# Kernel optimization log

Measured on AMD Instinct MI355X. Metric: run time of the kernel, lower is better.

## Reference

```python
import jax, jax.numpy as jnp
import numpy as np
from jax import lax

B, DIM, H, W = 16, 256, 32, 32
C = DIM // 4          # per-branch channels = 64
HEADS, DH = 8, 64
INNER = HEADS * DH    # 512
R = 16                # SE / CBAM channel reduction
PX = PY = 8           # learned param grid size


def _coords(n_in, n_out):
    s = jnp.linspace(0.0, n_in - 1.0, n_out)
    i0 = jnp.clip(jnp.floor(s).astype(jnp.int32), 0, max(n_in - 2, 0))
    return i0, jnp.clip(i0 + 1, 0, n_in - 1), s - i0


def resize_ac(p, out_h, out_w):
    # bilinear resize with align_corners=True; p: [..., h, w]
    y0, y1, fy = _coords(p.shape[-2], out_h)
    x0, x1, fx = _coords(p.shape[-1], out_w)
    py = p[..., y0, :] * (1.0 - fy)[:, None] + p[..., y1, :] * fy[:, None]
    return py[..., x0] * (1.0 - fx) + py[..., x1] * fx


def ln_last(x, w, b, eps=1e-5):  # torch nn.LayerNorm default eps
    m = x.mean(-1, keepdims=True)
    v = ((x - m) ** 2).mean(-1, keepdims=True)
    return (x - m) * lax.rsqrt(v + eps) * w + b


def ln_cf(x, w, b, eps=1e-6):  # channels_first ConvNeXt LayerNorm
    m = x.mean(1, keepdims=True)
    v = ((x - m) ** 2).mean(1, keepdims=True)
    return w[None, :, None, None] * ((x - m) * lax.rsqrt(v + eps)) + b[None, :, None, None]


def dwconv2d(x, w, b):  # depthwise 3x3, stride 1, pad 1
    o = lax.conv_general_dilated(x, w, (1, 1), 'SAME', dimension_numbers=('NCHW', 'OIHW', 'NCHW'), feature_group_count=x.shape[1])
    return o + b[None, :, None, None]


def dwconv1d(x, w, b):  # depthwise k=3, pad 1
    o = lax.conv_general_dilated(x, w, (1,), 'SAME', dimension_numbers=('NCH', 'OIH', 'NCH'), feature_group_count=x.shape[1])
    return o + b[None, :, None]


def pw(x, w, b):  # 1x1 conv over NCHW, w: [Cout, Cin]
    return jnp.einsum('bchw,dc->bdhw', x, w) + b[None, :, None, None]


def gelu(t):
    return jax.nn.gelu(t, approximate=False)  # torch nn.GELU default = erf


def attention(x, lnw, lnb, wqkv, wout):
    # x: [B, N, C]
    xn = ln_last(x, lnw, lnb)
    q, k, v = jnp.split(xn @ wqkv, 3, axis=-1)
    sp = lambda t: t.reshape(t.shape[0], t.shape[1], HEADS, DH).transpose(0, 2, 1, 3)
    q, k, v = sp(q), sp(k), sp(v)
    a = jax.nn.softmax(jnp.einsum('bhnd,bhmd->bhnm', q, k) * DH ** -0.5, axis=-1)
    o = jnp.einsum('bhnm,bhmd->bhnd', a, v).transpose(0, 2, 1, 3).reshape(x.shape[0], x.shape[1], INNER)
    return o @ wout


def cbam(x, fc1, fc2, sa_w):
    mlp = lambda t: jax.nn.relu(t @ fc1.T) @ fc2.T
    ca = jax.nn.sigmoid(mlp(x.mean((2, 3))) + mlp(x.max((2, 3))))
    x = x * ca[:, :, None, None]
    sp = jnp.stack([x.mean(1), x.max(1)], axis=1)  # [B,2,H,W]
    sa = lax.conv_general_dilated(sp, sa_w, (1, 1), 'SAME', dimension_numbers=('NCHW', 'OIHW', 'NCHW'))
    return x * jax.nn.sigmoid(sa)


def se(x, fc1, fc2):
    y = jax.nn.sigmoid(jax.nn.relu(x.mean((2, 3)) @ fc1.T) @ fc2.T)
    return x * y[:, :, None, None]


def setup_inputs() -> dict:
    key = jax.random.key(0)
    ks = iter(jax.random.split(key, 40))
    nrm = lambda shape, s=0.05: jax.random.normal(next(ks), shape, jnp.float32) * s
    d = {}
    d['x'] = jax.random.normal(next(ks), (B, DIM, H, W), jnp.float32)
    d['n1_w'] = jnp.ones((DIM,)); d['n1_b'] = jnp.zeros((DIM,))
    d['att_ln_w'] = jnp.ones((C,)); d['att_ln_b'] = jnp.zeros((C,))
    d['att_wqkv'] = nrm((C, 3 * INNER))
    d['att_wout'] = nrm((INNER, C))
    d['params_xy'] = jnp.ones((1, C, PX, PY))
    d['cxy_dw_w'] = nrm((C, 1, 3, 3)); d['cxy_dw_b'] = jnp.zeros((C,))
    d['cxy_pw_w'] = nrm((C, C)); d['cxy_pw_b'] = jnp.zeros((C,))
    d['ca_fc1'] = nrm((C // R, C)); d['ca_fc2'] = nrm((C, C // R))
    d['sa_w'] = nrm((1, 2, 7, 7))
    d['params_zx'] = jnp.ones((1, 1, C, PX))
    d['czx_dw_w'] = nrm((C, 1, 3)); d['czx_dw_b'] = jnp.zeros((C,))
    d['czx_pw_w'] = nrm((C, C)); d['czx_pw_b'] = jnp.zeros((C,))
    d['se_fc1'] = nrm((C // R, C)); d['se_fc2'] = nrm((C, C // R))
    d['params_zy'] = jnp.ones((1, 1, C, PY))
    d['czy_dw_w'] = nrm((C, 1, 3)); d['czy_dw_b'] = jnp.zeros((C,))
    d['czy_pw_w'] = nrm((C, C)); d['czy_pw_b'] = jnp.zeros((C,))
    d['dw_pw_w'] = nrm((C, C)); d['dw_pw_b'] = jnp.zeros((C,))
    d['dw_dw_w'] = nrm((C, 1, 3, 3)); d['dw_dw_b'] = jnp.zeros((C,))
    d['n2_w'] = jnp.ones((DIM,)); d['n2_b'] = jnp.zeros((DIM,))
    d['ldw_dw_w'] = nrm((DIM, 1, 3, 3)); d['ldw_dw_b'] = jnp.zeros((DIM,))
    d['ldw_pw_w'] = nrm((DIM, DIM)); d['ldw_pw_b'] = jnp.zeros((DIM,))
    return d


def reference(x, n1_w, n1_b, att_ln_w, att_ln_b, att_wqkv, att_wout, params_xy, cxy_dw_w, cxy_dw_b, cxy_pw_w, cxy_pw_b, ca_fc1, ca_fc2, sa_w, params_zx, czx_dw_w, czx_dw_b, czx_pw_w, czx_pw_b, se_fc1, se_fc2, params_zy, czy_dw_w, czy_dw_b, czy_pw_w, czy_pw_b, dw_pw_w, dw_pw_b, dw_dw_w, dw_dw_b, n2_w, n2_b, ldw_dw_w, ldw_dw_b, ldw_pw_w, ldw_pw_b):
    xn = ln_cf(x, n1_w, n1_b)
    x1, x2, x3, x4 = jnp.split(xn, 4, axis=1)
    Bz, Cz, Hz, Wz = x1.shape
    # branch 1: token self-attention, gated by conv'd upsampled learned grid
    t = attention(x1.transpose(0, 2, 3, 1).reshape(Bz, Hz * Wz, Cz), att_ln_w, att_ln_b, att_wqkv, att_wout)
    x1 = t.reshape(Bz, Hz, Wz, Cz).transpose(0, 3, 1, 2)
    g = pw(gelu(dwconv2d(resize_ac(params_xy, Hz, Wz), cxy_dw_w, cxy_dw_b)), cxy_pw_w, cxy_pw_b)
    x1 = x1 * g
    # branch 2: CBAM + zx gate (permute trick == broadcast over width)
    x2 = cbam(x2, ca_fc1, ca_fc2, sa_w)
    g = resize_ac(params_zx, Cz, Hz)[0]  # [1, C, H]
    g = jnp.einsum('bcl,dc->bdl', gelu(dwconv1d(g, czx_dw_w, czx_dw_b)), czx_pw_w) + czx_pw_b[None, :, None]
    x2 = x2 * g[:, :, :, None]
    # branch 3: SE + zy gate (broadcast over height)
    x3 = se(x3, se_fc1, se_fc2)
    g = resize_ac(params_zy, Cz, Wz)[0]  # [1, C, W]
    g = jnp.einsum('bcl,dc->bdl', gelu(dwconv1d(g, czy_dw_w, czy_dw_b)), czy_pw_w) + czy_pw_b[None, :, None]
    x3 = x3 * g[:, :, None, :]
    # branch 4: pointwise -> GELU -> depthwise
    x4 = dwconv2d(gelu(pw(x4, dw_pw_w, dw_pw_b)), dw_dw_w, dw_dw_b)
    out = ln_cf(jnp.concatenate([x1, x2, x3, x4], axis=1), n2_w, n2_b)
    return pw(gelu(dwconv2d(out, ldw_dw_w, ldw_dw_b)), ldw_pw_w, ldw_pw_b)
```

## Files before the change

### kernel.cpp

```cpp
#include <hip/hip_runtime.h>
#include <hip/hip_bf16.h>
#include <math.h>

#define B_     16
#define DIM_   256
#define H_     32
#define W_     32
#define HW_    1024
#define C_     64
#define HEADS_ 8
#define DH_    64
#define INNER_ 512
#define TOK_   16384

typedef unsigned short ushort_t;
typedef __bf16 bf16x8 __attribute__((ext_vector_type(8)));
typedef float  f32x4  __attribute__((ext_vector_type(4)));

#define AOFF_N1W     0
#define AOFF_N1B     256
#define AOFF_ALNW    512
#define AOFF_ALNB    576
#define AOFF_WQKV    640
#define AOFF_WOUT    98944
// ... 123 lines not shown
  int bb = pix >> 10, hw = pix & 1023;
  size_t base = (size_t)bb * (DIM_ * HW_) + hw;
  float s = 0.f, s2 = 0.f;
  for (int c = 0; c < 64; ++c) {
    float v = ldx(x, base + (size_t)(p * 64 + c) * HW_, xf);
    s += v; s2 += v * v;
  }
  ps[p][pi] = s; ps2[p][pi] = s2;
  __syncthreads();
  if (t < 64) {
    float S = ps[0][t] + ps[1][t] + ps[2][t] + ps[3][t];
    float S2 = ps2[0][t] + ps2[1][t] + ps2[2][t] + ps2[3][t];
    float mean = S * (1.0f / DIM_);
    float var = fmaxf(S2 * (1.0f / DIM_) - mean * mean, 0.f);
    int px = blockIdx.x * 64 + t;
    m1[px] = mean;
    r1[px] = rsqrtf(var + 1e-6f);
  }
}

__global__ __launch_bounds__(256) void k_ln_tok(const void* __restrict__ x, const int* __restrict__ dtf,
                                                const float* __restrict__ m1, const float* __restrict__ r1,
                                                const float* __restrict__ arena, ushort_t* __restrict__ x1ln,
                                                ushort_t* __restrict__ xn4) {
  __shared__ float ls[64 * 65];
  __shared__ float pm[4][64], pv[4][64];
  __shared__ float mt[64], rt[64];
  bool xf = dtf[0] != 0;
  int t = threadIdx.x;
  int bb = blockIdx.x >> 4, hw0 = (blockIdx.x & 15) * 64;
  #pragma unroll
  for (int i = 0; i < 16; ++i) {
    int ch = i * 4 + (t >> 6);
    int tk = t & 63;
    int tokg = bb * HW_ + hw0 + tk;
    float v = ldx(x, ((size_t)bb * DIM_ + ch) * HW_ + hw0 + tk, xf);
    ls[ch * 65 + tk] = (v - m1[tokg]) * r1[tokg] * arena[AOFF_N1W + ch] + arena[AOFF_N1B + ch];
  }
  __syncthreads();
  {
    int p = t >> 6, tk = t & 63;
    float s = 0.f, s2 = 0.f;
    #pragma unroll
    for (int c = 0; c < 16; ++c) {
      float v = ls[(p * 16 + c) * 65 + tk];
      s += v; s2 += v * v;
    }
    pm[p][tk] = s; pv[p][tk] = s2;
  }
  __syncthreads();
  if (t < 64) {
    float S = pm[0][t] + pm[1][t] + pm[2][t] + pm[3][t];
    float S2 = pv[0][t] + pv[1][t] + pv[2][t] + pv[3][t];
    float m = S * (1.0f / C_);
    float var = fmaxf(S2 * (1.0f / C_) - m * m, 0.f);
    mt[t] = m;
    rt[t] = rsqrtf(var + 1e-5f);
  }
  __syncthreads();
  {
    unsigned int* dst = (unsigned int*)x1ln;
    #pragma unroll
    for (int i = 0; i < 8; ++i) {
      int idx = i * 256 + t;
      int tok = idx >> 5, cp = idx & 31, c = cp * 2;
      float m = mt[tok], r = rt[tok];
      float v0 = (ls[c * 65 + tok] - m) * r * arena[AOFF_ALNW + c] + arena[AOFF_ALNB + c];
      float v1 = (ls[(c + 1) * 65 + tok] - m) * r * arena[AOFF_ALNW + c + 1] + arena[AOFF_ALNB + c + 1];
      int tokg = bb * HW_ + hw0 + tok;
      dst[(tokg * 64 + c) >> 1] = (unsigned int)f2us(v0) | ((unsigned int)f2us(v1) << 16);
    }
  }
  __syncthreads();
  #pragma unroll
  for (int i = 0; i < 16; ++i) {
    int ch = i * 4 + (t >> 6);
    int tk = t & 63;
    int tokg = bb * HW_ + hw0 + tk;
    float v = ldx(x, ((size_t)bb * DIM_ + 192 + ch) * HW_ + hw0 + tk, xf);
    ls[ch * 65 + tk] = (v - m1[tokg]) * r1[tokg] * arena[AOFF_N1W + 192 + ch] + arena[AOFF_N1B + 192 + ch];
  }
  __syncthreads();
  {
    unsigned int* dst = (unsigned int*)xn4;
    #pragma unroll
    for (int i = 0; i < 8; ++i) {
      int idx = i * 256 + t;
      int tok = idx >> 5, cp = idx & 31, c = cp * 2;
      float v0 = ls[c * 65 + tok];
      float v1 = ls[(c + 1) * 65 + tok];
      int tokg = bb * HW_ + hw0 + tok;
      dst[(tokg * 64 + c) >> 1] = (unsigned int)f2us(v0) | ((unsigned int)f2us(v1) << 16);
    }
  }
}

__global__ __launch_bounds__(256) void k_qkv_mfma(const ushort_t* __restrict__ x1ln,
                                                  const ushort_t* __restrict__ wqkvT,
                                                  ushort_t* __restrict__ q, ushort_t* __restrict__ k_,
                                                  ushort_t* __restrict__ v_, int tok_base) {
  int jc = blockIdx.x % 6;
  int mt = blockIdx.x / 6;
  int w = threadIdx.x >> 6, lane = threadIdx.x & 63;
  int m = lane & 15, quad = lane >> 4;
  int tok0 = mt * 64;
  bf16x8 a[4][2];
  #pragma unroll
  for (int s = 0; s < 4; ++s)
    #pragma unroll
    for (int kc = 0; kc < 2; ++kc)
      a[s][kc] = *(const bf16x8*)(x1ln + (size_t)(tok_base + tok0 + s*16 + m) * 64 + kc*32 + quad*8);
  bf16x8 bfr[4][2];
  #pragma unroll
  for (int nb = 0; nb < 4; ++nb)
    #pragma unroll
    for (int kc = 0; kc < 2; ++kc)
      bfr[nb][kc] = *(const bf16x8*)(wqkvT + (size_t)(jc*256 + w*64 + nb*16 + m) * 64 + kc*32 + quad*8);
  f32x4 cacc[4][4];
  #pragma unroll
  for (int s = 0; s < 4; ++s)
    #pragma unroll
    for (int nb = 0; nb < 4; ++nb) cacc[s][nb] = (f32x4){0.f, 0.f, 0.f, 0.f};
  #pragma unroll
  for (int kc = 0; kc < 2; ++kc)
    #pragma unroll
    for (int s = 0; s < 4; ++s)
      #pragma unroll
      for (int nb = 0; nb < 4; ++nb)
        cacc[s][nb] = __builtin_amdgcn_mfma_f32_16x16x32_bf16(a[s][kc], bfr[nb][kc], cacc[s][nb], 0, 0, 0);
  #pragma unroll
  for (int nb = 0; nb < 4; ++nb) {
    int j = jc*256 + w*64 + nb*16 + m;
    int which = j >> 9, jj = j & 511;
    int h = jj >> 6, d = jj & 63;
    ushort_t* dst = (which == 0) ? q : ((which == 1) ? k_ : v_);
    float sc = (which == 0) ? 0.125f : 1.0f;
    #pragma unroll
    for (int s = 0; s < 4; ++s)
      #pragma unroll
      for (int r = 0; r < 4; ++r) {
        int tl = tok0 + s*16 + quad*4 + r;
        int bl = tl >> 10, n = tl & 1023;
        dst[(((size_t)bl * HEADS_ + h) * 1024 + n) * 64 + d] = f2us(cacc[s][nb][r] * sc);
      }
  }
}

#define KSTR 72
__global__ __launch_bounds__(256) void k_flash_mfma(const ushort_t* __restrict__ q,
                                                    const ushort_t* __restrict__ k_,
                                                    const ushort_t* __restrict__ v_,
                                                    ushort_t* __restrict__ ao) {
  __shared__ ushort_t Kl[64 * KSTR];
  __shared__ ushort_t Vt[80 * KSTR];
  __shared__ ushort_t Pl[256 * KSTR];
  int bh = blockIdx.x >> 2;
  int qt = blockIdx.x & 3;
  int w = threadIdx.x >> 6, lane = threadIdx.x & 63;
  int m = lane & 15, quad = lane >> 4;
  const size_t bh_off = (size_t)bh * 1024 * 64;

  {
    unsigned int* vtp = (unsigned int*)&Vt[0];
    for (int i = threadIdx.x; i < 16 * (KSTR / 2); i += 256) {
      int row = i / (KSTR / 2);
      vtp[64 * (KSTR / 2) + i] = (row == 0) ? 0x3F803F80u : 0u;
    }
  }

  bf16x8 aq[4][2];
  #pragma unroll
  for (int s = 0; s < 4; ++s)
    #pragma unroll
    for (int kc = 0; kc < 2; ++kc)
      aq[s][kc] = *(const bf16x8*)(q + bh_off + (size_t)(qt*256 + w*64 + s*16 + m) * 64 + kc*32 + quad*8);

  f32x4 oacc[4][4];
  f32x4 lsum[4];
  #pragma unroll
  for (int s = 0; s < 4; ++s) {
    #pragma unroll
    for (int i = 0; i < 4; ++i) oacc[s][i] = (f32x4){0.f, 0.f, 0.f, 0.f};
    lsum[s] = (f32x4){0.f, 0.f, 0.f, 0.f};
  }

  __syncthreads();
  bf16x8 bvo0 = *(const bf16x8*)&Vt[(64 + m) * KSTR + quad*8];
  bf16x8 bvo1 = *(const bf16x8*)&Vt[(64 + m) * KSTR + 32 + quad*8];

  int kkey = threadIdx.x & 63;
  int kd0  = (threadIdx.x >> 6) * 16;
  int vkey = (threadIdx.x & 31) * 2;
  int vd0  = (threadIdx.x >> 5) * 8;

  for (int kt = 0; kt < 16; ++kt) {
    __syncthreads();
    {
      const uint4* src = (const uint4*)(k_ + bh_off + (size_t)(kt*64 + kkey)*64 + kd0);
      uint4 u0 = src[0], u1 = src[1];
      uint4* dst = (uint4*)&Kl[kkey * KSTR + kd0];
      dst[0] = u0; dst[1] = u1;
    }
    {
      const ushort4* s0 = (const ushort4*)(v_ + bh_off + (size_t)(kt*64 + vkey)*64 + vd0);
      const ushort4* s1 = (const ushort4*)(v_ + bh_off + (size_t)(kt*64 + vkey + 1)*64 + vd0);
      ushort4 x0 = s0[0], x1 = s0[1];
      ushort4 y0 = s1[0], y1 = s1[1];
      unsigned int* base = (unsigned int*)&Vt[0];
      int col = vkey >> 1;
      base[(vd0+0)*(KSTR/2) + col] = (unsigned int)x0.x | ((unsigned int)y0.x << 16);
      base[(vd0+1)*(KSTR/2) + col] = (unsigned int)x0.y | ((unsigned int)y0.y << 16);
      base[(vd0+2)*(KSTR/2) + col] = (unsigned int)x0.z | ((unsigned int)y0.z << 16);
      base[(vd0+3)*(KSTR/2) + col] = (unsigned int)x0.w | ((unsigned int)y0.w << 16);
      base[(vd0+4)*(KSTR/2) + col] = (unsigned int)x1.x | ((unsigned int)y1.x << 16);
      base[(vd0+5)*(KSTR/2) + col] = (unsigned int)x1.y | ((unsigned int)y1.y << 16);
      base[(vd0+6)*(KSTR/2) + col] = (unsigned int)x1.z | ((unsigned int)y1.z << 16);
      base[(vd0+7)*(KSTR/2) + col] = (unsigned int)x1.w | ((unsigned int)y1.w << 16);
    }
    __syncthreads();

    f32x4 sacc[4][4];
    #pragma unroll
    for (int s = 0; s < 4; ++s)
      #pragma unroll
      for (int kb = 0; kb < 4; ++kb) sacc[s][kb] = (f32x4){0.f, 0.f, 0.f, 0.f};
    #pragma unroll
    for (int kb = 0; kb < 4; ++kb) {
      bf16x8 bk0 = *(const bf16x8*)&Kl[(kb*16 + m) * KSTR + quad*8];
      bf16x8 bk1 = *(const bf16x8*)&Kl[(kb*16 + m) * KSTR + 32 + quad*8];
      #pragma unroll
      for (int s = 0; s < 4; ++s) {
        sacc[s][kb] = __builtin_amdgcn_mfma_f32_16x16x32_bf16(aq[s][0], bk0, sacc[s][kb], 0, 0, 0);
        sacc[s][kb] = __builtin_amdgcn_mfma_f32_16x16x32_bf16(aq[s][1], bk1, sacc[s][kb], 0, 0, 0);
      }
    }

    #pragma unroll
    for (int s = 0; s < 4; ++s) {
      #pragma unroll
      for (int kb = 0; kb < 4; ++kb) {
        float p0 = __expf(fminf(sacc[s][kb][0], 30.f));
        float p1 = __expf(fminf(sacc[s][kb][1], 30.f));
        float p2 = __expf(fminf(sacc[s][kb][2], 30.f));
        float p3 = __expf(fminf(sacc[s][kb][3], 30.f));
        int rbase = (w*64 + s*16 + quad*4) * KSTR + kb*16 + m;
        Pl[rbase + 0*KSTR] = f2us(p0);
        Pl[rbase + 1*KSTR] = f2us(p1);
        Pl[rbase + 2*KSTR] = f2us(p2);
        Pl[rbase + 3*KSTR] = f2us(p3);
      }
    }

    bf16x8 ap[4][2];
    #pragma unroll
    for (int s = 0; s < 4; ++s)
      #pragma unroll
      for (int kc = 0; kc < 2; ++kc)
        ap[s][kc] = *(const bf16x8*)&Pl[(w*64 + s*16 + m) * KSTR + kc*32 + quad*8];
    #pragma unroll
    for (int db = 0; db < 4; ++db) {
      bf16x8 bv0 = *(const bf16x8*)&Vt[(db*16 + m) * KSTR + quad*8];
      bf16x8 bv1 = *(const bf16x8*)&Vt[(db*16 + m) * KSTR + 32 + quad*8];
      #pragma unroll
      for (int s = 0; s < 4; ++s) {
        oacc[s][db] = __builtin_amdgcn_mfma_f32_16x16x32_bf16(ap[s][0], bv0, oacc[s][db], 0, 0, 0);
        oacc[s][db] = __builtin_amdgcn_mfma_f32_16x16x32_bf16(ap[s][1], bv1, oacc[s][db], 0, 0, 0);
      }
    }
    #pragma unroll
    for (int s = 0; s < 4; ++s) {
      lsum[s] = __builtin_amdgcn_mfma_f32_16x16x32_bf16(ap[s][0], bvo0, lsum[s], 0, 0, 0);
      lsum[s] = __builtin_amdgcn_mfma_f32_16x16x32_bf16(ap[s][1], bvo1, lsum[s], 0, 0, 0);
    }
  }

  int bl = bh >> 3, h = bh & 7;
  int srcl = lane & 48;
  #pragma unroll
  for (int s = 0; s < 4; ++s) {
    #pragma unroll
    for (int r = 0; r < 4; ++r) {
      float l = __shfl(lsum[s][r], srcl, 64);
      float inv = 1.0f / l;
      int qrow = qt*256 + w*64 + s*16 + quad*4 + r;
      ushort_t* op = ao + ((size_t)(bl*1024 + qrow)) * INNER_ + h*64 + m;
      #pragma unroll
      for (int db = 0; db < 4; ++db) op[db*16] = f2us(oacc[s][db][r] * inv);
    }
  }
}

__global__ __launch_bounds__(256) void k_outproj_mfma(const ushort_t* __restrict__ ao,
                                                      const ushort_t* __restrict__ woutT,
                                                      const float* __restrict__ g1,
                                                      ushort_t* __restrict__ cat, int tok_base) {
  int w = threadIdx.x >> 6, lane = threadIdx.x & 63;
  int m = lane & 15, quad = lane >> 4;
  int tok0 = blockIdx.x * 64 + w * 16;
  f32x4 cacc[4];
  #pragma unroll
  for (int nb = 0; nb < 4; ++nb) cacc[nb] = (f32x4){0.f, 0.f, 0.f, 0.f};
  for (int kc = 0; kc < 16; ++kc) {
    bf16x8 a = *(const bf16x8*)(ao + (size_t)(tok0 + m) * INNER_ + kc*32 + quad*8);
    #pragma unroll
    for (int nb = 0; nb < 4; ++nb) {
      bf16x8 b = *(const bf16x8*)(woutT + (size_t)(nb*16 + m) * INNER_ + kc*32 + quad*8);
      cacc[nb] = __builtin_amdgcn_mfma_f32_16x16x32_bf16(a, b, cacc[nb], 0, 0, 0);
    }
  }
  #pragma unroll
  for (int nb = 0; nb < 4; ++nb) {
    int c = nb*16 + m;
    #pragma unroll
    for (int r = 0; r < 4; ++r) {
      int tokg = tok_base + tok0 + quad*4 + r;
      int bb = tokg >> 10, hw = tokg & 1023;
      cat[((size_t)bb * DIM_ + c) * HW_ + hw] = f2us(cacc[nb][r] * g1[c * HW_ + hw]);
    }
  }
}

__global__ void k_dwg_xy(const float* __restrict__ arena, float* __restrict__ t1) {
  const float* w = arena + AOFF_CXYDW;
  const float* b = arena + AOFF_CXYDWB;
  int idx = blockIdx.x * 256 + threadIdx.x;
  int c = idx >> 10, hw = idx & 1023, yy = hw >> 5, xx = hw & 31;
  const float* pc = arena + AOFF_PXY + c * 64;
  float acc = b[c];
  #pragma unroll
  for (int ky = 0; ky < 3; ++ky) {
    int ny = yy + ky - 1; if (ny < 0 || ny > 31) continue;
    float sy = ny * (7.0f / 31.0f); int y0 = (int)floorf(sy); y0 = y0 > 6 ? 6 : y0; float fy = sy - y0;
    #pragma unroll
    for (int kx = 0; kx < 3; ++kx) {
      int nx = xx + kx - 1; if (nx < 0 || nx > 31) continue;
      float sx = nx * (7.0f / 31.0f); int x0 = (int)floorf(sx); x0 = x0 > 6 ? 6 : x0; float fx = sx - x0;
      float a  = pc[y0*8+x0] * (1.f-fy) + pc[(y0+1)*8+x0] * fy;
      float b2 = pc[y0*8+x0+1] * (1.f-fy) + pc[(y0+1)*8+x0+1] * fy;
      acc += w[c*9 + ky*3 + kx] * (a * (1.f - fx) + b2 * fx);
    }
  }
  t1[idx] = gelu_f(acc);
}
__global__ void k_pw_xy(const float* __restrict__ t1, const float* __restrict__ arena,
                        float* __restrict__ g1) {
  const float* w = arena + AOFF_CXYPW;
  const float* b = arena + AOFF_CXYPWB;
  int idx = blockIdx.x * 256 + threadIdx.x;
  int d = idx >> 10, hw = idx & 1023;
  float acc = b[d];
  for (int c = 0; c < C_; ++c) acc += w[d*C_ + c] * t1[c*HW_ + hw];
  g1[idx] = acc;
}

__global__ __launch_bounds__(256) void k_gate_full(const float* __restrict__ arena,
                                                   float* __restrict__ g2, float* __restrict__ g3) {
  __shared__ float ts[C_ * 32];
  int gi = blockIdx.x;
  int po  = gi ? AOFF_PZY   : AOFF_PZX;
  int wo  = gi ? AOFF_CZYDW : AOFF_CZXDW;
  int bo  = gi ? AOFF_CZYDWB: AOFF_CZXDWB;
  int pwo = gi ? AOFF_CZYPW : AOFF_CZXPW;
  int pbo = gi ? AOFF_CZYPWB: AOFF_CZXPWB;
  float* g = gi ? g3 : g2;
  const float* p   = arena + po;
  const float* dww = arena + wo;
  const float* dwb = arena + bo;
  for (int idx = threadIdx.x; idx < C_ * 32; idx += 256) {
    int c = idx >> 5, i = idx & 31;
    float acc = dwb[c];
    #pragma unroll
    for (int kk = 0; kk < 3; ++kk) {
      int ii = i + kk - 1;
      if (ii < 0 || ii > 31) continue;
      float s = ii * (7.0f / 31.0f); int x0 = (int)floorf(s); x0 = x0 > 6 ? 6 : x0; float f = s - x0;
      float val = p[c*8 + x0] * (1.f - f) + p[c*8 + x0 + 1] * f;
      acc += dww[c*3 + kk] * val;
    }
    ts[idx] = gelu_f(acc);
  }
  __syncthreads();
  const float* w = arena + pwo;
  const float* b = arena + pbo;
  for (int idx = threadIdx.x; idx < C_ * 32; idx += 256) {
    int d = idx >> 5, i = idx & 31;
    float acc = b[d];
    for (int c = 0; c < C_; ++c) acc += w[d*C_ + c] * ts[c*32 + i];
    g[idx] = acc;
  }
}

__global__ __launch_bounds__(256) void k_pool2(const void* __restrict__ x, const int* __restrict__ dtf,
                                               const float* __restrict__ m1, const float* __restrict__ r1,
                                               const float* __restrict__ arena,
                                               float* __restrict__ camean, float* __restrict__ camax,
                                               float* __restrict__ sem, float* __restrict__ semx) {
  __shared__ float sm[256], sx[256];
  bool xf = dtf[0] != 0;
  int which = blockIdx.x >> 10;
  int blk = blockIdx.x & 1023;
  int coff = which ? 128 : 64;
  float* om = which ? sem  : camean;
  float* ox = which ? semx : camax;
  int bb = blk >> 6, c = blk & 63;
  const size_t xbase = ((size_t)bb * DIM_ + coff + c) * HW_;
  const float* mb = m1 + bb * HW_;
  const float* rb = r1 + bb * HW_;
  float wc = arena[AOFF_N1W + coff + c], bc = arena[AOFF_N1B + coff + c];
  int tid = threadIdx.x;
  float s = 0.f, mx = -1e30f;
  for (int i = tid; i < HW_; i += 256) {
    float v = (ldx(x, xbase + i, xf) - mb[i]) * rb[i] * wc + bc;
    s += v; mx = fmaxf(mx, v);
  }
  sm[tid] = s; sx[tid] = mx; __syncthreads();
  for (int st = 128; st > 0; st >>= 1) {
    if (tid < st) { sm[tid] += sm[tid+st]; sx[tid] = fmaxf(sx[tid], sx[tid+st]); }
    __syncthreads();
  }
  if (tid == 0) { om[blk] = sm[0] * (1.0f / HW_); ox[blk] = sx[0]; }
}

__global__ void k_ca_mlp(const float* __restrict__ mean, const float* __restrict__ mx,
                         const float* __restrict__ arena, float* __restrict__ ca) {
  __shared__ float hid[8];
  const float* fc1 = arena + AOFF_CAF1;
  const float* fc2 = arena + AOFF_CAF2;
  int bb = blockIdx.x, tid = threadIdx.x;
  if (tid < 8) {
    int which = tid >> 2, r = tid & 3;
    const float* src = which ? mx : mean;
    float s = 0.f;
    for (int c = 0; c < C_; ++c) s += src[bb*C_ + c] * fc1[r*C_ + c];
    hid[tid] = fmaxf(s, 0.f);
  }
  __syncthreads();
  float s = 0.f;
  #pragma unroll
  for (int r = 0; r < 4; ++r) s += (hid[r] + hid[4+r]) * fc2[tid*4 + r];
  ca[bb*C_ + tid] = sigmoid_f(s);
}

__global__ void k_se_mlp(const float* __restrict__ mean, const float* __restrict__ arena,
                         float* __restrict__ se) {
  __shared__ float hid[4];
  const float* fc1 = arena + AOFF_SEF1;
  const float* fc2 = arena + AOFF_SEF2;
  int bb = blockIdx.x, tid = threadIdx.x;
  if (tid < 4) {
    float s = 0.f;
    for (int c = 0; c < C_; ++c) s += mean[bb*C_ + c] * fc1[tid*C_ + c];
    hid[tid] = fmaxf(s, 0.f);
  }
  __syncthreads();
  float s = 0.f;
  #pragma unroll
  for (int r = 0; r < 4; ++r) s += hid[r] * fc2[tid*4 + r];
  se[bb*C_ + tid] = sigmoid_f(s);
}

__global__ __launch_bounds__(256) void k_spmaps(const void* __restrict__ x, const int* __restrict__ dtf,
                                                const float* __restrict__ m1, const float* __restrict__ r1,
                                                const float* __restrict__ arena, const float* __restrict__ ca,
                                                float* __restrict__ spm, float* __restrict__ spx) {
  __shared__ float ps[4][64], px[4][64];
  bool xf = dtf[0] != 0;
  int t = threadIdx.x;
  int pi = t & 63, p = t >> 6;
  int pix = blockIdx.x * 64 + pi;
  int bb = pix >> 10, hw = pix & 1023;
  float m = m1[pix], r = r1[pix];
  float s = 0.f, mx = -1e30f;
  for (int c = 0; c < 16; ++c) {
    int ch = p * 16 + c;
    float v = (ldx(x, ((size_t)bb * DIM_ + 64 + ch) * HW_ + hw, xf) - m) * r * arena[AOFF_N1W + 64 + ch] + arena[AOFF_N1B + 64 + ch];
    v *= ca[bb*C_ + ch];
    s += v; mx = fmaxf(mx, v);
  }
  ps[p][pi] = s; px[p][pi] = mx;
  __syncthreads();
  if (t < 64) {
    float S = ps[0][t] + ps[1][t] + ps[2][t] + ps[3][t];
    float M = fmaxf(fmaxf(px[0][t], px[1][t]), fmaxf(px[2][t], px[3][t]));
    int pxi = blockIdx.x * 64 + t;
    spm[pxi] = S * (1.0f / C_);
    spx[pxi] = M;
  }
}

__global__ void k_saconv(const float* __restrict__ spm, const float* __restrict__ spx,
                         const float* __restrict__ arena, float* __restrict__ samask) {
  const float* w = arena + AOFF_SAW;
  int idx = blockIdx.x * 256 + threadIdx.x;
  int bb = idx >> 10, hw = idx & 1023, yy = hw >> 5, xx = hw & 31;
  float acc = 0.f;
  for (int ky = 0; ky < 7; ++ky) {
    int ny = yy + ky - 3; if (ny < 0 || ny > 31) continue;
    for (int kx = 0; kx < 7; ++kx) {
      int nx = xx + kx - 3; if (nx < 0 || nx > 31) continue;
      int off = bb*HW_ + ny*32 + nx;
      acc += spm[off] * w[ky*7 + kx] + spx[off] * w[49 + ky*7 + kx];
    }
  }
  samask[idx] = sigmoid_f(acc);
}

__global__ void k_bfin(const void* __restrict__ x, const int* __restrict__ dtf,
                       const float* __restrict__ m1, const float* __restrict__ r1,
                       const float* __restrict__ arena,
                       const float* __restrict__ ca, const float* __restrict__ samask,
                       const float* __restrict__ g2,
                       const float* __restrict__ se, const float* __restrict__ g3,
                       ushort_t* __restrict__ cat) {
  bool xf = dtf[0] != 0;
  bool second = blockIdx.x >= 4096;
  int idx = ((int)blockIdx.x & 4095) * 256 + threadIdx.x;
  int hw = idx & 1023, tmp = idx >> 10, c = tmp & 63, bb = tmp >> 6;
  int t = bb * HW_ + hw;
  if (!second) {
    int h = hw >> 5;
    size_t o = ((size_t)bb * DIM_ + 64 + c) * HW_ + hw;
    float v = (ldx(x, o, xf) - m1[t]) * r1[t] * arena[AOFF_N1W + 64 + c] + arena[AOFF_N1B + 64 + c];
    cat[o] = f2us(v * ca[bb*C_ + c] * samask[t] * g2[c*32 + h]);
  } else {
    size_t o = ((size_t)bb * DIM_ + 128 + c) * HW_ + hw;
    float v = (ldx(x, o, xf) - m1[t]) * r1[t] * arena[AOFF_N1W + 128 + c] + arena[AOFF_N1B + 128 + c];
    cat[o] = f2us(v * se[bb*C_ + c] * g3[c*32 + (hw & 31)]);
  }
}

__global__ __launch_bounds__(256) void k_b4_mfma(const ushort_t* __restrict__ xn4,
                                                 const ushort_t* __restrict__ wdw,
                                                 const float* __restrict__ arena,
                                                 ushort_t* __restrict__ t4) {
  int w = threadIdx.x >> 6, lane = threadIdx.x & 63;
  int m = lane & 15, quad = lane >> 4;
  int tok0 = blockIdx.x * 64 + w * 16;
  bf16x8 a0 = *(const bf16x8*)(xn4 + (size_t)(tok0 + m) * 64 + quad*8);
  bf16x8 a1 = *(const bf16x8*)(xn4 + (size_t)(tok0 + m) * 64 + 32 + quad*8);
  f32x4 cacc[4];
  #pragma unroll
  for (int nb = 0; nb < 4; ++nb) cacc[nb] = (f32x4){0.f, 0.f, 0.f, 0.f};
  #pragma unroll
  for (int nb = 0; nb < 4; ++nb) {
    bf16x8 b0 = *(const bf16x8*)(wdw + (size_t)(nb*16 + m) * 64 + quad*8);
    bf16x8 b1 = *(const bf16x8*)(wdw + (size_t)(nb*16 + m) * 64 + 32 + quad*8);
    cacc[nb] = __builtin_amdgcn_mfma_f32_16x16x32_bf16(a0, b0, cacc[nb], 0, 0, 0);
    cacc[nb] = __builtin_amdgcn_mfma_f32_16x16x32_bf16(a1, b1, cacc[nb], 0, 0, 0);
  }
  #pragma unroll
  for (int nb = 0; nb < 4; ++nb) {
    int cout = nb*16 + m;
    float bv = arena[AOFF_DWPWB + cout];
    #pragma unroll
    for (int r = 0; r < 4; ++r) {
      int tokg = tok0 + quad*4 + r;
      int bb = tokg >> 10, hw = tokg & 1023;
      t4[((size_t)bb * C_ + cout) * HW_ + hw] = f2us(gelu_f(cacc[nb][r] + bv));
    }
  }
}
__global__ void k_b4_dw(const ushort_t* __restrict__ t4, const float* __restrict__ arena,
                        ushort_t* __restrict__ cat) {
  const float* w = arena + AOFF_DWDW;
  int idx = blockIdx.x * 256 + threadIdx.x;
  int hw = idx & 1023, tmp = idx >> 10, c = tmp & 63, bb = tmp >> 6;
  int yy = hw >> 5, xx = hw & 31;
  const ushort_t* base = t4 + ((size_t)bb * C_ + c) * HW_;
  float acc = arena[AOFF_DWDWB + c];
  #pragma unroll
  for (int ky = 0; ky < 3; ++ky) {
    int ny = yy + ky - 1; if (ny < 0 || ny > 31) continue;
    #pragma unroll
    for (int kx = 0; kx < 3; ++kx) {
      int nx = xx + kx - 1; if (nx < 0 || nx > 31) continue;
      acc += w[c*9 + ky*3 + kx] * us2f(base[ny*32 + nx]);
    }
  }
  cat[((size_t)bb * DIM_ + 192 + c) * HW_ + hw] = f2us(acc);
}

__global__ __launch_bounds__(256) void k_ln2norm(ushort_t* __restrict__ cat) {
  __shared__ float ps[4][64], ps2[4][64];
  __shared__ float mS[64], rS[64];
  int t = threadIdx.x;
  int pi = t & 63, p = t >> 6;
  int pix = blockIdx.x * 64 + pi;
  int bb = pix >> 10, hw = pix & 1023;
  size_t base = (size_t)bb * (DIM_ * HW_) + hw;
  float v[64];
  float s = 0.f, s2 = 0.f;
  #pragma unroll
  for (int c = 0; c < 64; ++c) {
    v[c] = us2f(cat[base + (size_t)(p * 64 + c) * HW_]);
    s += v[c]; s2 += v[c] * v[c];
  }
  ps[p][pi] = s; ps2[p][pi] = s2;
  __syncthreads();
  if (t < 64) {
    float S = ps[0][t] + ps[1][t] + ps[2][t] + ps[3][t];
    float S2 = ps2[0][t] + ps2[1][t] + ps2[2][t] + ps2[3][t];
    float mean = S * (1.0f / DIM_);
    float var = fmaxf(S2 * (1.0f / DIM_) - mean * mean, 0.f);
    mS[t] = mean;
    rS[t] = rsqrtf(var + 1e-6f);
  }
  __syncthreads();
  float mean = mS[pi], rr = rS[pi];
  #pragma unroll
  for (int c = 0; c < 64; ++c)
    cat[base + (size_t)(p * 64 + c) * HW_] = f2us((v[c] - mean) * rr);
}

__global__ void k_final_dw(const ushort_t* __restrict__ cat, const float* __restrict__ arena,
                           ushort_t* __restrict__ z) {
  const float* w = arena + AOFF_LDWDW;
  int idx = blockIdx.x * 256 + threadIdx.x;
  int hw = idx & 1023, tmp = idx >> 10, cc = tmp & 255, bb = tmp >> 8;
  int yy = hw >> 5, xx = hw & 31;
  const ushort_t* base = cat + ((size_t)bb * DIM_ + cc) * HW_;
  float wcc = arena[AOFF_N2W + cc], bcc = arena[AOFF_N2B + cc];
  float sumws = 0.f, sumw = 0.f;
  #pragma unroll
  for (int ky = 0; ky < 3; ++ky) {
    int ny = yy + ky - 1; if (ny < 0 || ny > 31) continue;
    #pragma unroll
    for (int kx = 0; kx < 3; ++kx) {
      int nx = xx + kx - 1; if (nx < 0 || nx > 31) continue;
      float wk = w[cc*9 + ky*3 + kx];
      sumws += wk * us2f(base[ny*32 + nx]);
      sumw  += wk;
    }
  }
  float acc = arena[AOFF_LDWDWB + cc] + wcc * sumws + bcc * sumw;
  z[((size_t)bb * DIM_ + cc) * HW_ + hw] = f2us(gelu_f(acc));
}

#define ZSTR 264
__global__ __launch_bounds__(256) void k_final_pw_mfma(const ushort_t* __restrict__ z,
                                                       const ushort_t* __restrict__ wpw,
                                                       const float* __restrict__ arena,
                                                       const int* __restrict__ dtf,
                                                       void* __restrict__ out) {
  __shared__ ushort_t zt[64 * ZSTR];
  bool of = dtf[0] != 0;
  int bb = blockIdx.x >> 4, hw0 = (blockIdx.x & 15) * 64;
  int t = threadIdx.x;
  int w = t >> 6, lane = t & 63;
  int m = lane & 15, quad = lane >> 4;
  #pragma unroll
  for (int i = 0; i < 4; ++i) {
    int cp = i * 32 + (t >> 3);
    int c = cp * 2;
    int hw8 = (t & 7) * 8;
    const ushort4* s0 = (const ushort4*)(z + ((size_t)bb * DIM_ + c) * HW_ + hw0 + hw8);
    const ushort4* s1 = (const ushort4*)(z + ((size_t)bb * DIM_ + c + 1) * HW_ + hw0 + hw8);
    ushort4 x0 = s0[0], x1 = s0[1];
    ushort4 y0 = s1[0], y1 = s1[1];
    unsigned int* basep = (unsigned int*)zt;
    basep[(hw8+0)*(ZSTR/2) + cp] = (unsigned int)x0.x | ((unsigned int)y0.x << 16);
    basep[(hw8+1)*(ZSTR/2) + cp] = (unsigned int)x0.y | ((unsigned int)y0.y << 16);
    basep[(hw8+2)*(ZSTR/2) + cp] = (unsigned int)x0.z | ((unsigned int)y0.z << 16);
    basep[(hw8+3)*(ZSTR/2) + cp] = (unsigned int)x0.w | ((unsigned int)y0.w << 16);
    basep[(hw8+4)*(ZSTR/2) + cp] = (unsigned int)x1.x | ((unsigned int)y1.x << 16);
    basep[(hw8+5)*(ZSTR/2) + cp] = (unsigned int)x1.y | ((unsigned int)y1.y << 16);
    basep[(hw8+6)*(ZSTR/2) + cp] = (unsigned int)x1.z | ((unsigned int)y1.z << 16);
    basep[(hw8+7)*(ZSTR/2) + cp] = (unsigned int)x1.w | ((unsigned int)y1.w << 16);
  }
  __syncthreads();
  f32x4 cacc[4][4];
  #pragma unroll
  for (int s = 0; s < 4; ++s)
    #pragma unroll
    for (int nb = 0; nb < 4; ++nb) cacc[s][nb] = (f32x4){0.f, 0.f, 0.f, 0.f};
  for (int kc = 0; kc < 8; ++kc) {
    bf16x8 a[4], b[4];
    #pragma unroll
    for (int s = 0; s < 4; ++s)
      a[s] = *(const bf16x8*)(wpw + (size_t)(w*64 + s*16 + m) * DIM_ + kc*32 + quad*8);
    #pragma unroll
    for (int nb = 0; nb < 4; ++nb)
      b[nb] = *(const bf16x8*)&zt[(nb*16 + m) * ZSTR + kc*32 + quad*8];
    #pragma unroll
    for (int s = 0; s < 4; ++s)
      #pragma unroll
      for (int nb = 0; nb < 4; ++nb)
        cacc[s][nb] = __builtin_amdgcn_mfma_f32_16x16x32_bf16(a[s], b[nb], cacc[s][nb], 0, 0, 0);
  }
  #pragma unroll
  for (int s = 0; s < 4; ++s) {
    #pragma unroll
    for (int r = 0; r < 4; ++r) {
      int d = w*64 + s*16 + quad*4 + r;
      float bv = arena[AOFF_LDWPWB + d];
      #pragma unroll
      for (int nb = 0; nb < 4; ++nb) {
        int hw = hw0 + nb*16 + m;
        float v = cacc[s][nb][r] + bv;
        size_t o = ((size_t)bb * DIM_ + d) * HW_ + hw;
        if (of) ((float*)out)[o] = v; else ((ushort_t*)out)[o] = f2us(v);
      }
    }
  }
}

extern "C" void kernel_launch(void* const* d_in, const int* in_sizes, int n_in,
                              void* d_out, int out_size, void* d_ws, size_t ws_size,
                              hipStream_t stream) {
  const void* x = d_in[0];

  char* wsp = (char*)d_ws; size_t off = 0;
  auto alloc = [&](size_t bytes) -> void* { void* p = wsp + off; off += (bytes + 255) & ~(size_t)255; return p; };

  int*      dtf   = (int*)alloc(sizeof(int));
  float*    arena = (float*)alloc(sizeof(float) * ATOTAL);
  ushort_t* wqkvT = (ushort_t*)alloc(2ull * 1536 * 64);
  ushort_t* woutT = (ushort_t*)alloc(2ull * 64 * 512);
  ushort_t* wpwB  = (ushort_t*)alloc(2ull * DIM_ * DIM_);
  ushort_t* wdwpwB= (ushort_t*)alloc(2ull * C_ * C_);
  ushort_t* x1ln  = (ushort_t*)alloc(2ull * TOK_ * C_);
  ushort_t* xn4   = (ushort_t*)alloc(2ull * TOK_ * C_);
  float*    g1    = (float*)alloc(sizeof(float) * C_ * HW_);
  float*    g2    = (float*)alloc(sizeof(float) * C_ * 32);
  float*    g3    = (float*)alloc(sizeof(float) * C_ * 32);
  float*    camean= (float*)alloc(sizeof(float) * B_ * C_);
  float*    camax = (float*)alloc(sizeof(float) * B_ * C_);
  float*    cab   = (float*)alloc(sizeof(float) * B_ * C_);
  float*    sem   = (float*)alloc(sizeof(float) * B_ * C_);
  float*    semx  = (float*)alloc(sizeof(float) * B_ * C_);
  float*    seb   = (float*)alloc(sizeof(float) * B_ * C_);
  float*    spm   = (float*)alloc(sizeof(float) * B_ * HW_);
  float*    spx   = (float*)alloc(sizeof(float) * B_ * HW_);
  float*    sam   = (float*)alloc(sizeof(float) * B_ * HW_);
  float*    m1    = (float*)alloc(sizeof(float) * TOK_);
  float*    r1    = (float*)alloc(sizeof(float) * TOK_);

  const size_t qkv_pb  = 2ull * HEADS_ * 1024 * 64;
  const size_t ao_pb   = 2ull * 1024 * INNER_;
  const size_t z_bytes = 2ull * B_ * DIM_ * HW_;
  size_t remain = (ws_size > off) ? (ws_size - off) : 0;
  int bs = 0;
  for (int cand = B_; cand >= 1; cand >>= 1) {
    size_t need = (size_t)cand * (3 * qkv_pb + ao_pb);
    if (need < z_bytes) need = z_bytes;
    if (need + 65536 <= remain) { bs = cand; break; }
  }
  if (bs == 0) {
    k_probe<<<1, 256, 0, stream>>>((const ushort_t*)x, dtf);
    k_diag<<<16384, 256, 0, stream>>>(d_out, dtf, 100.0f + (float)(ws_size >> 20));
    return;
  }
  const int nsplit = B_ / bs;
  size_t qsz = (size_t)bs * qkv_pb;
  size_t region_bytes = (size_t)bs * (3 * qkv_pb + ao_pb);
  if (region_bytes < z_bytes) region_bytes = z_bytes;
  char* region = (char*)alloc(region_bytes);
  float*    t1xy = (float*)(region);
  ushort_t* qq   = (ushort_t*)(region);
  ushort_t* kk   = (ushort_t*)(region + qsz);
  ushort_t* vv   = (ushort_t*)(region + 2 * qsz);
  ushort_t* aob  = (ushort_t*)(region + 3 * qsz);
  ushort_t* t4   = (ushort_t*)(region);
  ushort_t* zbuf = (ushort_t*)(region);
  ushort_t* cat  = (ushort_t*)d_out;

  k_probe<<<1, 256, 0, stream>>>((const ushort_t*)x, dtf);
  k_cvt_all<<<(ATOTAL + 255) / 256, 256, 0, stream>>>(
      d_in[1], d_in[2], d_in[3], d_in[4], d_in[5], d_in[6], d_in[7], d_in[8], d_in[9],
      d_in[10], d_in[11], d_in[12], d_in[13], d_in[14], d_in[15], d_in[16], d_in[17], d_in[18],
      d_in[19], d_in[20], d_in[21], d_in[22], d_in[23], d_in[24], d_in[25], d_in[26], d_in[27],
      d_in[28], d_in[29], d_in[30], d_in[31], d_in[32], d_in[33], d_in[34], d_in[35], d_in[36],
      dtf, arena);
  k_wprep<<<784, 256, 0, stream>>>(arena, wqkvT, woutT, wpwB, wdwpwB);

  k_ln1stats<<<256, 256, 0, stream>>>(x, dtf, m1, r1);
  k_ln_tok<<<256, 256, 0, stream>>>(x, dtf, m1, r1, arena, x1ln, xn4);

  k_dwg_xy<<<256, 256, 0, stream>>>(arena, t1xy);
  k_pw_xy<<<256, 256, 0, stream>>>(t1xy, arena, g1);
  k_gate_full<<<2, 256, 0, stream>>>(arena, g2, g3);

  for (int si = 0; si < nsplit; ++si) {
    int tok_base = si * bs * 1024;
    k_qkv_mfma<<<bs * 96, 256, 0, stream>>>(x1ln, wqkvT, qq, kk, vv, tok_base);
    k_flash_mfma<<<bs * HEADS_ * 4, 256, 0, stream>>>(qq, kk, vv, aob);
    k_outproj_mfma<<<bs * 16, 256, 0, stream>>>(aob, woutT, g1, cat, tok_base);
  }

  k_pool2<<<2048, 256, 0, stream>>>(x, dtf, m1, r1, arena, camean, camax, sem, semx);
  k_ca_mlp<<<16, 64, 0, stream>>>(camean, camax, arena, cab);
  k_se_mlp<<<16, 64, 0, stream>>>(sem, arena, seb);
  k_spmaps<<<256, 256, 0, stream>>>(x, dtf, m1, r1, arena, cab, spm, spx);
  k_saconv<<<64, 256, 0, stream>>>(spm, spx, arena, sam);
  k_bfin<<<8192, 256, 0, stream>>>(x, dtf, m1, r1, arena, cab, sam, g2, seb, g3, cat);

  k_b4_mfma<<<256, 256, 0, stream>>>(xn4, wdwpwB, arena, t4);
  k_b4_dw<<<4096, 256, 0, stream>>>(t4, arena, cat);

  k_ln2norm<<<256, 256, 0, stream>>>(cat);
  k_final_dw<<<16384, 256, 0, stream>>>(cat, arena, zbuf);
  k_final_pw_mfma<<<256, 256, 0, stream>>>(zbuf, wpwB, arena, dtf, d_out);
}
```

Before: 437.9 us.

## Replace MFMA row-sum with shuffle reduction; fuse gate and channel-MLP kernels

The flash-attention kernel now computes softmax row sums with per-lane accumulation and xor-shuffle reductions instead of extra MFMAs against a ones column. That removes the Vt padding rows and the init barrier, but adds shuffle work inside the loop. Separately, the xy gate depthwise and pointwise kernels are fused into one 16-block kernel that keeps the intermediate in shared memory. The CA and SE MLP kernels are merged into a single launch. The fused gate kernel uses far fewer blocks, which may serialize work that previously spread across the GPU.

After: 462.8 us. 1.06x slower.

```diff
diff --git a/kernel.cpp b/kernel.cpp
--- a/kernel.cpp
+++ b/kernel.cpp
@@ -299,7 +299,7 @@
                                                     const ushort_t* __restrict__ v_,
                                                     ushort_t* __restrict__ ao) {
   __shared__ ushort_t Kl[64 * KSTR];
-  __shared__ ushort_t Vt[80 * KSTR];
+  __shared__ ushort_t Vt[64 * KSTR];
   __shared__ ushort_t Pl[256 * KSTR];
   int bh = blockIdx.x >> 2;
   int qt = blockIdx.x & 3;
@@ -307,14 +307,6 @@
   int m = lane & 15, quad = lane >> 4;
   const size_t bh_off = (size_t)bh * 1024 * 64;
 
-  {
-    unsigned int* vtp = (unsigned int*)&Vt[0];
-    for (int i = threadIdx.x; i < 16 * (KSTR / 2); i += 256) {
-      int row = i / (KSTR / 2);
-      vtp[64 * (KSTR / 2) + i] = (row == 0) ? 0x3F803F80u : 0u;
-    }
-  }
-
   bf16x8 aq[4][2];
   #pragma unroll
   for (int s = 0; s < 4; ++s)
@@ -323,17 +315,14 @@
       aq[s][kc] = *(const bf16x8*)(q + bh_off + (size_t)(qt*256 + w*64 + s*16 + m) * 64 + kc*32 + quad*8);
 
   f32x4 oacc[4][4];
-  f32x4 lsum[4];
-  #pragma unroll
-  for (int s = 0; s < 4; ++s) {
-    #pragma unroll
-    for (int i = 0; i < 4; ++i) oacc[s][i] = (f32x4){0.f, 0.f, 0.f, 0.f};
-    lsum[s] = (f32x4){0.f, 0.f, 0.f, 0.f};
-  }
-
-  __syncthreads();
-  bf16x8 bvo0 = *(const bf16x8*)&Vt[(64 + m) * KSTR + quad*8];
-  bf16x8 bvo1 = *(const bf16x8*)&Vt[(64 + m) * KSTR + 32 + quad*8];
+  float lacc[4][4];
+  #pragma unroll
+  for (int s = 0; s < 4; ++s)
+    #pragma unroll
+    for (int i = 0; i < 4; ++i) {
+      oacc[s][i] = (f32x4){0.f, 0.f, 0.f, 0.f};
+      lacc[s][i] = 0.f;
+    }
 
   int kkey = threadIdx.x & 63;
   int kd0  = (threadIdx.x >> 6) * 16;
@@ -384,18 +373,28 @@
 
     #pragma unroll
     for (int s = 0; s < 4; ++s) {
+      float rs0 = 0.f, rs1 = 0.f, rs2 = 0.f, rs3 = 0.f;
       #pragma unroll
       for (int kb = 0; kb < 4; ++kb) {
         float p0 = __expf(fminf(sacc[s][kb][0], 30.f));
         float p1 = __expf(fminf(sacc[s][kb][1], 30.f));
         float p2 = __expf(fminf(sacc[s][kb][2], 30.f));
         float p3 = __expf(fminf(sacc[s][kb][3], 30.f));
+        rs0 += p0; rs1 += p1; rs2 += p2; rs3 += p3;
         int rbase = (w*64 + s*16 + quad*4) * KSTR + kb*16 + m;
         Pl[rbase + 0*KSTR] = f2us(p0);
         Pl[rbase + 1*KSTR] = f2us(p1);
         Pl[rbase + 2*KSTR] = f2us(p2);
         Pl[rbase + 3*KSTR] = f2us(p3);
       }
+      #pragma unroll
+      for (int mask = 1; mask <= 8; mask <<= 1) {
+        rs0 += __shfl_xor(rs0, mask, 64);
+        rs1 += __shfl_xor(rs1, mask, 64);
+        rs2 += __shfl_xor(rs2, mask, 64);
+        rs3 += __shfl_xor(rs3, mask, 64);
+      }
+      lacc[s][0] += rs0; lacc[s][1] += rs1; lacc[s][2] += rs2; lacc[s][3] += rs3;
     }
 
     bf16x8 ap[4][2];
@@ -414,21 +413,14 @@
         oacc[s][db] = __builtin_amdgcn_mfma_f32_16x16x32_bf16(ap[s][1], bv1, oacc[s][db], 0, 0, 0);
       }
     }
-    #pragma unroll
-    for (int s = 0; s < 4; ++s) {
-      lsum[s] = __builtin_amdgcn_mfma_f32_16x16x32_bf16(ap[s][0], bvo0, lsum[s], 0, 0, 0);
-      lsum[s] = __builtin_amdgcn_mfma_f32_16x16x32_bf16(ap[s][1], bvo1, lsum[s], 0, 0, 0);
-    }
   }
 
   int bl = bh >> 3, h = bh & 7;
-  int srcl = lane & 48;
   #pragma unroll
   for (int s = 0; s < 4; ++s) {
     #pragma unroll
     for (int r = 0; r < 4; ++r) {
-      float l = __shfl(lsum[s][r], srcl, 64);
-      float inv = 1.0f / l;
+      float inv = 1.0f / lacc[s][r];
       int qrow = qt*256 + w*64 + s*16 + quad*4 + r;
       ushort_t* op = ao + ((size_t)(bl*1024 + qrow)) * INNER_ + h*64 + m;
       #pragma unroll
@@ -467,37 +459,47 @@
   }
 }
 
-__global__ void k_dwg_xy(const float* __restrict__ arena, float* __restrict__ t1) {
+__global__ __launch_bounds__(256) void k_gate_xy(const float* __restrict__ arena,
+                                                 float* __restrict__ g1) {
+  __shared__ float ts[C_ * 64];
+  int t = threadIdx.x;
+  int hw0 = blockIdx.x * 64;
   const float* w = arena + AOFF_CXYDW;
   const float* b = arena + AOFF_CXYDWB;
-  int idx = blockIdx.x * 256 + threadIdx.x;
-  int c = idx >> 10, hw = idx & 1023, yy = hw >> 5, xx = hw & 31;
-  const float* pc = arena + AOFF_PXY + c * 64;
-  float acc = b[c];
-  #pragma unroll
-  for (int ky = 0; ky < 3; ++ky) {
-    int ny = yy + ky - 1; if (ny < 0 || ny > 31) continue;
-    float sy = ny * (7.0f / 31.0f); int y0 = (int)floorf(sy); y0 = y0 > 6 ? 6 : y0; float fy = sy - y0;
-    #pragma unroll
-    for (int kx = 0; kx < 3; ++kx) {
-      int nx = xx + kx - 1; if (nx < 0 || nx > 31) continue;
-      float sx = nx * (7.0f / 31.0f); int x0 = (int)floorf(sx); x0 = x0 > 6 ? 6 : x0; float fx = sx - x0;
-      float a  = pc[y0*8+x0] * (1.f-fy) + pc[(y0+1)*8+x0] * fy;
-      float b2 = pc[y0*8+x0+1] * (1.f-fy) + pc[(y0+1)*8+x0+1] * fy;
-      acc += w[c*9 + ky*3 + kx] * (a * (1.f - fx) + b2 * fx);
-    }
-  }
-  t1[idx] = gelu_f(acc);
-}
-__global__ void k_pw_xy(const float* __restrict__ t1, const float* __restrict__ arena,
-                        float* __restrict__ g1) {
-  const float* w = arena + AOFF_CXYPW;
-  const float* b = arena + AOFF_CXYPWB;
-  int idx = blockIdx.x * 256 + threadIdx.x;
-  int d = idx >> 10, hw = idx & 1023;
-  float acc = b[d];
-  for (int c = 0; c < C_; ++c) acc += w[d*C_ + c] * t1[c*HW_ + hw];
-  g1[idx] = acc;
+  #pragma unroll
+  for (int i = 0; i < 16; ++i) {
+    int e = i * 256 + t;
+    int c = e >> 6, hwl = e & 63;
+    int hw = hw0 + hwl;
+    int yy = hw >> 5, xx = hw & 31;
+    const float* pc = arena + AOFF_PXY + c * 64;
+    float acc = b[c];
+    #pragma unroll
+    for (int ky = 0; ky < 3; ++ky) {
+      int ny = yy + ky - 1; if (ny < 0 || ny > 31) continue;
+      float sy = ny * (7.0f / 31.0f); int y0 = (int)floorf(sy); y0 = y0 > 6 ? 6 : y0; float fy = sy - y0;
+      #pragma unroll
+      for (int kx = 0; kx < 3; ++kx) {
+        int nx = xx + kx - 1; if (nx < 0 || nx > 31) continue;
+        float sx = nx * (7.0f / 31.0f); int x0 = (int)floorf(sx); x0 = x0 > 6 ? 6 : x0; float fx = sx - x0;
+        float a  = pc[y0*8+x0] * (1.f-fy) + pc[(y0+1)*8+x0] * fy;
+        float b2 = pc[y0*8+x0+1] * (1.f-fy) + pc[(y0+1)*8+x0+1] * fy;
+        acc += w[c*9 + ky*3 + kx] * (a * (1.f - fx) + b2 * fx);
+      }
+    }
+    ts[c * 64 + hwl] = gelu_f(acc);
+  }
+  __syncthreads();
+  const float* wp = arena + AOFF_CXYPW;
+  const float* bp = arena + AOFF_CXYPWB;
+  #pragma unroll
+  for (int i = 0; i < 16; ++i) {
+    int e = i * 256 + t;
+    int d = e >> 6, hwl = e & 63;
+    float acc = bp[d];
+    for (int c = 0; c < C_; ++c) acc += wp[d*C_ + c] * ts[c*64 + hwl];
+    g1[d * HW_ + hw0 + hwl] = acc;
+  }
 }
 
 __global__ __launch_bounds__(256) void k_gate_full(const float* __restrict__ arena,
@@ -568,42 +570,41 @@
   if (tid == 0) { om[blk] = sm[0] * (1.0f / HW_); ox[blk] = sx[0]; }
 }
 
-__global__ void k_ca_mlp(const float* __restrict__ mean, const float* __restrict__ mx,
-                         const float* __restrict__ arena, float* __restrict__ ca) {
+__global__ void k_chmlp(const float* __restrict__ camean, const float* __restrict__ camax,
+                        const float* __restrict__ sem, const float* __restrict__ arena,
+                        float* __restrict__ ca, float* __restrict__ se) {
   __shared__ float hid[8];
-  const float* fc1 = arena + AOFF_CAF1;
-  const float* fc2 = arena + AOFF_CAF2;
-  int bb = blockIdx.x, tid = threadIdx.x;
-  if (tid < 8) {
-    int which = tid >> 2, r = tid & 3;
-    const float* src = which ? mx : mean;
+  int which = blockIdx.x >> 4;
+  int bb = blockIdx.x & 15, tid = threadIdx.x;
+  if (!which) {
+    const float* fc1 = arena + AOFF_CAF1;
+    const float* fc2 = arena + AOFF_CAF2;
+    if (tid < 8) {
+      int half = tid >> 2, r = tid & 3;
+      const float* src = half ? camax : camean;
+      float s = 0.f;
+      for (int c = 0; c < C_; ++c) s += src[bb*C_ + c] * fc1[r*C_ + c];
+      hid[tid] = fmaxf(s, 0.f);
+    }
+    __syncthreads();
     float s = 0.f;
-    for (int c = 0; c < C_; ++c) s += src[bb*C_ + c] * fc1[r*C_ + c];
-    hid[tid] = fmaxf(s, 0.f);
-  }
-  __syncthreads();
-  float s = 0.f;
-  #pragma unroll
-  for (int r = 0; r < 4; ++r) s += (hid[r] + hid[4+r]) * fc2[tid*4 + r];
-  ca[bb*C_ + tid] = sigmoid_f(s);
-}
-
-__global__ void k_se_mlp(const float* __restrict__ mean, const float* __restrict__ arena,
-                         float* __restrict__ se) {
-  __shared__ float hid[4];
-  const float* fc1 = arena + AOFF_SEF1;
-  const float* fc2 = arena + AOFF_SEF2;
-  int bb = blockIdx.x, tid = threadIdx.x;
-  if (tid < 4) {
+    #pragma unroll
+    for (int r = 0; r < 4; ++r) s += (hid[r] + hid[4+r]) * fc2[tid*4 + r];
+    ca[bb*C_ + tid] = sigmoid_f(s);
+  } else {
+    const float* fc1 = arena + AOFF_SEF1;
+    const float* fc2 = arena + AOFF_SEF2;
+    if (tid < 4) {
+      float s = 0.f;
+      for (int c = 0; c < C_; ++c) s += sem[bb*C_ + c] * fc1[tid*C_ + c];
+      hid[tid] = fmaxf(s, 0.f);
+    }
+    __syncthreads();
     float s = 0.f;
-    for (int c = 0; c < C_; ++c) s += mean[bb*C_ + c] * fc1[tid*C_ + c];
-    hid[tid] = fmaxf(s, 0.f);
-  }
-  __syncthreads();
-  float s = 0.f;
-  #pragma unroll
-  for (int r = 0; r < 4; ++r) s += hid[r] * fc2[tid*4 + r];
-  se[bb*C_ + tid] = sigmoid_f(s);
+    #pragma unroll
+    for (int r = 0; r < 4; ++r) s += hid[r] * fc2[tid*4 + r];
+    se[bb*C_ + tid] = sigmoid_f(s);
+  }
 }
 
 __global__ __launch_bounds__(256) void k_spmaps(const void* __restrict__ x, const int* __restrict__ dtf,
@@ -902,7 +903,6 @@
   size_t region_bytes = (size_t)bs * (3 * qkv_pb + ao_pb);
   if (region_bytes < z_bytes) region_bytes = z_bytes;
   char* region = (char*)alloc(region_bytes);
-  float*    t1xy = (float*)(region);
   ushort_t* qq   = (ushort_t*)(region);
   ushort_t* kk   = (ushort_t*)(region + qsz);
   ushort_t* vv   = (ushort_t*)(region + 2 * qsz);
@@ -923,8 +923,7 @@
   k_ln1stats<<<256, 256, 0, stream>>>(x, dtf, m1, r1);
   k_ln_tok<<<256, 256, 0, stream>>>(x, dtf, m1, r1, arena, x1ln, xn4);
 
-  k_dwg_xy<<<256, 256, 0, stream>>>(arena, t1xy);
-  k_pw_xy<<<256, 256, 0, stream>>>(t1xy, arena, g1);
+  k_gate_xy<<<16, 256, 0, stream>>>(arena, g1);
   k_gate_full<<<2, 256, 0, stream>>>(arena, g2, g3);
 
   for (int si = 0; si < nsplit; ++si) {
@@ -935,8 +934,7 @@
   }
 
   k_pool2<<<2048, 256, 0, stream>>>(x, dtf, m1, r1, arena, camean, camax, sem, semx);
-  k_ca_mlp<<<16, 64, 0, stream>>>(camean, camax, arena, cab);
-  k_se_mlp<<<16, 64, 0, stream>>>(sem, arena, seb);
+  k_chmlp<<<32, 64, 0, stream>>>(camean, camax, sem, arena, cab, seb);
   k_spmaps<<<256, 256, 0, stream>>>(x, dtf, m1, r1, arena, cab, spm, spx);
   k_saconv<<<64, 256, 0, stream>>>(spm, spx, arena, sam);
   k_bfin<<<8192, 256, 0, stream>>>(x, dtf, m1, r1, arena, cab, sam, g2, seb, g3, cat);
```
